# Kernel tuning notes

Measured on AMD Instinct MI355X. Metric: run time of the kernel, lower is better.

## Reference

```python
import jax, jax.numpy as jnp
import numpy as np

N, S, R, CM = 1, 128, 256, 256
C, CZ = 32, 128


def setup_inputs() -> dict:
    key = jax.random.key(0)
    k1, k2, k3, k4 = jax.random.split(key, 4)
    return {
        "msa_repr": jax.random.normal(k1, (N, S, R, CM), dtype=jnp.float32),
        "left_proj": jax.random.normal(k2, (CM, C), dtype=jnp.float32) * 0.05,
        "right_proj": jax.random.normal(k3, (CM, C), dtype=jnp.float32) * 0.05,
        "out_proj": jax.random.normal(k4, (C * C, CZ), dtype=jnp.float32) * 0.05,
    }


def reference(msa_repr, left_proj, right_proj, out_proj):
    # msa_repr: [N, S, R, CM]
    # Project to left/right activations and move R before S
    # (equivalent to torch matmul + transpose(-2, -3)).
    a = jnp.einsum("nsrm,mc->nrsc", msa_repr, left_proj)   # [N, R, S, C]
    b = jnp.einsum("nsrm,mc->nrsc", msa_repr, right_proj)  # [N, R, S, C]
    # Outer product contracted over the MSA dim S:
    # outer[n, r, t, c, e] = sum_s a[n, r, s, c] * b[n, t, s, e]
    outer = jnp.einsum("nrsc,ntse->nrtce", a, b)            # [N, R, R, C, C]
    n, r, t = outer.shape[:3]
    outer = outer.reshape(n, r, t, C * C)                   # [N, R, R, C*C]
    # Output projection to pair channels cz
    return outer @ out_proj                                 # [N, R, R, CZ]
```

## Files before the change

kernel.cpp:

```cpp
#include <hip/hip_runtime.h>

typedef __bf16 bf16x8 __attribute__((ext_vector_type(8)));
typedef __bf16 bf16x4 __attribute__((ext_vector_type(4)));
typedef float f32x16 __attribute__((ext_vector_type(16)));

constexpr int S = 128, R = 256, CM = 256, C = 32, CZ = 128;

#define MFMA __builtin_amdgcn_mfma_f32_32x32x16_bf16

__device__ __forceinline__ bf16x4 cvt4(float a, float b, float c, float d) {
    bf16x4 r;
    r[0] = (__bf16)a; r[1] = (__bf16)b; r[2] = (__bf16)c; r[3] = (__bf16)d;
    return r;
}

__global__ __launch_bounds__(256) void k_wt(const float* __restrict__ W,
                                            __bf16* __restrict__ WTf) {
    int g = blockIdx.x * 256 + threadIdx.x;
    int cz = g & 127;
    int k = g >> 7;
    int e = k >> 5, c = k & 31;
    float v = W[(size_t)(c * 32 + e) * 128 + cz];
    WTf[((size_t)(k >> 3) * 128 + cz) * 8 + (k & 7)] = (__bf16)v;
}

__global__ __launch_bounds__(256) void k_wlr(const float* __restrict__ Lp,
                                             const float* __restrict__ Rp,
                                             __bf16* __restrict__ WLRT) {
    int c = blockIdx.x;
    int m = threadIdx.x;
    const float* src = (c < 32) ? Lp : Rp;
    WLRT[(size_t)c * 256 + m] = (__bf16)src[(size_t)m * 32 + (c & 31)];
}

__global__ __launch_bounds__(256) void k_proj(const float* __restrict__ msa,
                                              const __bf16* __restrict__ WLRT,
                                              __bf16* __restrict__ aTf,
                                              __bf16* __restrict__ bTf) {
    __shared__ __align__(16) __bf16 As[128 * 256];
    const int r = blockIdx.x;
    const int t = threadIdx.x;
    const int w = t >> 6;
    const int lane = t & 63;

#pragma unroll 4
    for (int it = 0; it < 32; ++it) {
        int row = it * 4 + w;
        float4 v = *(const float4*)&msa[((size_t)row * R + r) * CM + lane * 4];
        bf16x4 h = cvt4(v.x, v.y, v.z, v.w);
        int P = (lane >> 1) ^ (row & 15);
        *(bf16x4*)((char*)As + row * 512 + P * 16 + (lane & 1) * 8) = h;
    }
    __syncthreads();

    const int l31 = t & 31;
    const int kh = (t >> 5) & 1;
    f32x16 accL, accR;
#pragma unroll
    for (int q = 0; q < 16; ++q) { accL[q] = 0.f; accR[q] = 0.f; }

    const bf16x8* wbL = (const bf16x8*)&WLRT[(size_t)l31 * 256 + 8 * kh];
    const bf16x8* wbR = (const bf16x8*)&WLRT[(size_t)(32 + l31) * 256 + 8 * kh];
    const int srow = w * 32 + l31;
    const char* arow = (const char*)As + srow * 512;

    __builtin_amdgcn_s_setprio(1);
#pragma unroll
    for (int ks = 0; ks < 16; ++ks) {
        int P = (2 * ks + kh) ^ (srow & 15);
        bf16x8 af = *(const bf16x8*)(arow + P * 16);
        accL = MFMA(af, wbL[2 * ks], accL, 0, 0, 0);
        accR = MFMA(af, wbR[2 * ks], accR, 0, 0, 0);
    }
    __builtin_amdgcn_s_setprio(0);

#pragma unroll
    for (int q = 0; q < 4; ++q) {
        size_t base = (size_t)r * 4096 + (size_t)(2 * w + (q >> 1)) * 512 +
                      (size_t)(q & 1) * 256 + (size_t)l31 * 8 + 4 * kh;
        *(bf16x4*)&aTf[base] = cvt4(accL[4 * q + 0], accL[4 * q + 1],
                                    accL[4 * q + 2], accL[4 * q + 3]);
        *(bf16x4*)&bTf[base] = cvt4(accR[4 * q + 0], accR[4 * q + 1],
                                    accR[4 * q + 2], accR[4 * q + 3]);
    }
}

__global__ __launch_bounds__(256, 2) void k_main(const __bf16* __restrict__ aTf,
                                                 const __bf16* __restrict__ bTf,
                                                 const __bf16* __restrict__ WTf,
                                                 float* __restrict__ out) {
    __shared__ __align__(16) __bf16 Gs[32 * 1024];

    const int t = threadIdx.x;
    const int w = t >> 6;
    const int l = t & 63;
    const int lane = l & 31;
    const int kh = l >> 5;
    const int r0 = blockIdx.x * 8;
    const int t0 = blockIdx.y * 4;

    f32x16 acc[2][4];
#pragma unroll
    for (int i = 0; i < 2; ++i)
#pragma unroll
        for (int j = 0; j < 4; ++j)
#pragma unroll
            for (int q = 0; q < 16; ++q) acc[i][j][q] = 0.f;

    const bf16x8* ap0 = (const bf16x8*)aTf + ((size_t)(r0 + 2 * w + 0) * 512 + kh * 32 + lane);
    const bf16x8* ap1 = (const bf16x8*)aTf + ((size_t)(r0 + 2 * w + 1) * 512 + kh * 32 + lane);
    const bf16x8* bp0 = (const bf16x8*)bTf + ((size_t)(t0 + 0) * 512 + kh * 32 + lane);
    const bf16x8* bp1 = (const bf16x8*)bTf + ((size_t)(t0 + 1) * 512 + kh * 32 + lane);
    const bf16x8* bp2 = (const bf16x8*)bTf + ((size_t)(t0 + 2) * 512 + kh * 32 + lane);
    const bf16x8* bp3 = (const bf16x8*)bTf + ((size_t)(t0 + 3) * 512 + kh * 32 + lane);

    bf16x8 A0[2], B0[4], A1[2], B1[4], A2[2], B2[4];
#define LDA(Aa, Bb, ks) do { \
    Aa[0] = ap0[(ks) * 64]; Aa[1] = ap1[(ks) * 64]; \
    Bb[0] = bp0[(ks) * 64]; Bb[1] = bp1[(ks) * 64]; \
    Bb[2] = bp2[(ks) * 64]; Bb[3] = bp3[(ks) * 64]; } while (0)
#define PH_A(Aa, Bb) do { \
    __builtin_amdgcn_s_setprio(1); \
    acc[0][0] = MFMA(Aa[0], Bb[0], acc[0][0], 0, 0, 0); \
    acc[0][1] = MFMA(Aa[0], Bb[1], acc[0][1], 0, 0, 0); \
    acc[0][2] = MFMA(Aa[0], Bb[2], acc[0][2], 0, 0, 0); \
    acc[0][3] = MFMA(Aa[0], Bb[3], acc[0][3], 0, 0, 0); \
    acc[1][0] = MFMA(Aa[1], Bb[0], acc[1][0], 0, 0, 0); \
    acc[1][1] = MFMA(Aa[1], Bb[1], acc[1][1], 0, 0, 0); \
    acc[1][2] = MFMA(Aa[1], Bb[2], acc[1][2], 0, 0, 0); \
    acc[1][3] = MFMA(Aa[1], Bb[3], acc[1][3], 0, 0, 0); \
    __builtin_amdgcn_s_setprio(0); } while (0)

    LDA(A0, B0, 0); LDA(A1, B1, 1); LDA(A2, B2, 2);
    PH_A(A0, B0); LDA(A0, B0, 3);
    PH_A(A1, B1); LDA(A1, B1, 4);
    PH_A(A2, B2); LDA(A2, B2, 5);
    PH_A(A0, B0); LDA(A0, B0, 6);
    PH_A(A1, B1); LDA(A1, B1, 7);
    PH_A(A2, B2);
    PH_A(A0, B0);
    PH_A(A1, B1);

#pragma unroll
    for (int i = 0; i < 2; ++i) {
#pragma unroll
        for (int j = 0; j < 4; ++j) {
            int p = (2 * w + i) * 4 + j;
            unsigned prow = (unsigned)p * 2048;
#pragma unroll
            for (int q = 0; q < 4; ++q) {
                int Lc = lane * 4 + q;
                int P = Lc ^ (p & 15) ^ (lane & 7);
                *(bf16x4*)((char*)Gs + prow + (unsigned)P * 16 + kh * 8) =
                    cvt4(acc[i][j][4 * q + 0], acc[i][j][4 * q + 1],
                         acc[i][j][4 * q + 2], acc[i][j][4 * q + 3]);
            }
        }
    }
    __syncthreads();

    f32x16 oA, oB;
#pragma unroll
    for (int q = 0; q < 16; ++q) { oA[q] = 0.f; oB[q] = 0.f; }

    const int czl = w * 32 + lane;
    const bf16x8* wb = (const bf16x8*)WTf + ((size_t)kh * 128 + czl);
    const unsigned prow = (unsigned)lane * 2048;
    const int p15 = lane & 15;

#define LDG1(dst, kk) do { \
    int Lr = (kk) * 2 + kh; \
    int P = Lr ^ p15 ^ ((Lr >> 2) & 7); \
    dst = *(const bf16x8*)((const char*)Gs + prow + (unsigned)P * 16); } while (0)

    bf16x8 G0[8], G1[8], W0[8], W1[8], W2[8];
#define LDG8(Gg, kb) do { \
    LDG1(Gg[0], (kb) + 0); LDG1(Gg[1], (kb) + 1); LDG1(Gg[2], (kb) + 2); LDG1(Gg[3], (kb) + 3); \
    LDG1(Gg[4], (kb) + 4); LDG1(Gg[5], (kb) + 5); LDG1(Gg[6], (kb) + 6); LDG1(Gg[7], (kb) + 7); } while (0)
#define LDW8(Ww, kb) do { \
    Ww[0] = wb[((kb) + 0) * 256]; Ww[1] = wb[((kb) + 1) * 256]; \
    Ww[2] = wb[((kb) + 2) * 256]; Ww[3] = wb[((kb) + 3) * 256]; \
    Ww[4] = wb[((kb) + 4) * 256]; Ww[5] = wb[((kb) + 5) * 256]; \
    Ww[6] = wb[((kb) + 6) * 256]; Ww[7] = wb[((kb) + 7) * 256]; } while (0)
#define PH_B(Gg, Ww) do { \
    __builtin_amdgcn_s_setprio(1); \
    oA = MFMA(Gg[0], Ww[0], oA, 0, 0, 0); oB = MFMA(Gg[1], Ww[1], oB, 0, 0, 0); \
    oA = MFMA(Gg[2], Ww[2], oA, 0, 0, 0); oB = MFMA(Gg[3], Ww[3], oB, 0, 0, 0); \
    oA = MFMA(Gg[4], Ww[4], oA, 0, 0, 0); oB = MFMA(Gg[5], Ww[5], oB, 0, 0, 0); \
    oA = MFMA(Gg[6], Ww[6], oA, 0, 0, 0); oB = MFMA(Gg[7], Ww[7], oB, 0, 0, 0); \
    __builtin_amdgcn_s_setprio(0); } while (0)

    LDW8(W0, 0); LDW8(W1, 8); LDW8(W2, 16);
    LDG8(G0, 0); LDG8(G1, 8);
    PH_B(G0, W0); LDW8(W0, 24); LDG8(G0, 16);
    PH_B(G1, W1); LDW8(W1, 32); LDG8(G1, 24);
    PH_B(G0, W2); LDW8(W2, 40); LDG8(G0, 32);
    PH_B(G1, W0); LDW8(W0, 48); LDG8(G1, 40);
    PH_B(G0, W1); LDW8(W1, 56); LDG8(G0, 48);
    PH_B(G1, W2);                LDG8(G1, 56);
    PH_B(G0, W0);
    PH_B(G1, W1);

    f32x16 o = oA + oB;

#pragma unroll
    for (int reg = 0; reg < 16; ++reg) {
        int p = (reg & 3) + 8 * (reg >> 2) + 4 * kh;
        int pr = p >> 2, pt = p & 3;
        out[((size_t)(r0 + pr) * 256 + (t0 + pt)) * 128 + czl] = o[reg];
    }
}

extern "C" void kernel_launch(void* const* d_in, const int* in_sizes, int n_in,
                              void* d_out, int out_size, void* d_ws, size_t ws_size,
                              hipStream_t stream) {
    const float* msa = (const float*)d_in[0];
    const float* left = (const float*)d_in[1];
    const float* right = (const float*)d_in[2];
    const float* W = (const float*)d_in[3];

    __bf16* aTf = (__bf16*)d_ws;
    __bf16* bTf = aTf + (size_t)R * 4096;
    __bf16* WTf = bTf + (size_t)R * 4096;
    __bf16* WLRT = WTf + (size_t)128 * 1024;
    float* outp = (float*)d_out;

    k_wt<<<512, 256, 0, stream>>>(W, WTf);
    k_wlr<<<64, 256, 0, stream>>>(left, right, WLRT);
    k_proj<<<256, 256, 0, stream>>>(msa, WLRT, aTf, bTf);
    k_main<<<dim3(32, 64), 256, 0, stream>>>(aTf, bTf, WTf, outp);
}
```

Measured before the change: 67.20 us.

## Enlarge main tile to 8x8 pairs with split-K output projection and LDS reduction

k_main now uses 512-thread blocks covering 8 r by 8 t pairs, which halves the grid and reuses each loaded a row across twice as many t columns. The output projection is split over K across wave pairs, each wave computing a 2x2 block of 32x32 MFMA tiles, and the partial sums are combined through an fp32 LDS reduction. k_proj is split across two S halves so it launches twice as many blocks, each computing a single projection per wave. The aim is more reuse of the W and G operands and better parallelism, at the cost of more LDS traffic and extra barriers for the reduction.

```diff
diff --git a/kernel.cpp b/kernel.cpp
--- a/kernel.cpp
+++ b/kernel.cpp
@@ -3,6 +3,7 @@
 typedef __bf16 bf16x8 __attribute__((ext_vector_type(8)));
 typedef __bf16 bf16x4 __attribute__((ext_vector_type(4)));
 typedef float f32x16 __attribute__((ext_vector_type(16)));
+typedef float f32x4 __attribute__((ext_vector_type(4)));
 
 constexpr int S = 128, R = 256, CM = 256, C = 32, CZ = 128;
 
@@ -37,31 +38,35 @@
                                               const __bf16* __restrict__ WLRT,
                                               __bf16* __restrict__ aTf,
                                               __bf16* __restrict__ bTf) {
-    __shared__ __align__(16) __bf16 As[128 * 256];
+    __shared__ __align__(16) __bf16 As[64 * 256];
     const int r = blockIdx.x;
+    const int sh = blockIdx.y;
     const int t = threadIdx.x;
+
+#pragma unroll 4
+    for (int it = 0; it < 16; ++it) {
+        int idx = it * 256 + t;
+        int row = idx >> 6;
+        int cg = idx & 63;
+        float4 v = *(const float4*)&msa[((size_t)(sh * 64 + row) * R + r) * CM + cg * 4];
+        bf16x4 h = cvt4(v.x, v.y, v.z, v.w);
+        int P = (cg >> 1) ^ (row & 15);
+        *(bf16x4*)((char*)As + row * 512 + P * 16 + (cg & 1) * 8) = h;
+    }
+    __syncthreads();
+
     const int w = t >> 6;
-    const int lane = t & 63;
-
-#pragma unroll 4
-    for (int it = 0; it < 32; ++it) {
-        int row = it * 4 + w;
-        float4 v = *(const float4*)&msa[((size_t)row * R + r) * CM + lane * 4];
-        bf16x4 h = cvt4(v.x, v.y, v.z, v.w);
-        int P = (lane >> 1) ^ (row & 15);
-        *(bf16x4*)((char*)As + row * 512 + P * 16 + (lane & 1) * 8) = h;
-    }
-    __syncthreads();
-
     const int l31 = t & 31;
     const int kh = (t >> 5) & 1;
-    f32x16 accL, accR;
-#pragma unroll
-    for (int q = 0; q < 16; ++q) { accL[q] = 0.f; accR[q] = 0.f; }
-
-    const bf16x8* wbL = (const bf16x8*)&WLRT[(size_t)l31 * 256 + 8 * kh];
-    const bf16x8* wbR = (const bf16x8*)&WLRT[(size_t)(32 + l31) * 256 + 8 * kh];
-    const int srow = w * 32 + l31;
+    const int sd = w & 1;
+    const int mi = w >> 1;
+
+    f32x16 acc;
+#pragma unroll
+    for (int q = 0; q < 16; ++q) acc[q] = 0.f;
+
+    const bf16x8* wb = (const bf16x8*)&WLRT[(size_t)(sd * 32 + l31) * 256 + 8 * kh];
+    const int srow = mi * 32 + l31;
     const char* arow = (const char*)As + srow * 512;
 
     __builtin_amdgcn_s_setprio(1);
@@ -69,27 +74,26 @@
     for (int ks = 0; ks < 16; ++ks) {
         int P = (2 * ks + kh) ^ (srow & 15);
         bf16x8 af = *(const bf16x8*)(arow + P * 16);
-        accL = MFMA(af, wbL[2 * ks], accL, 0, 0, 0);
-        accR = MFMA(af, wbR[2 * ks], accR, 0, 0, 0);
+        acc = MFMA(af, wb[2 * ks], acc, 0, 0, 0);
     }
     __builtin_amdgcn_s_setprio(0);
 
+    __bf16* dst = sd ? bTf : aTf;
+    const int wg = sh * 2 + mi;
 #pragma unroll
     for (int q = 0; q < 4; ++q) {
-        size_t base = (size_t)r * 4096 + (size_t)(2 * w + (q >> 1)) * 512 +
+        size_t base = (size_t)r * 4096 + (size_t)(2 * wg + (q >> 1)) * 512 +
                       (size_t)(q & 1) * 256 + (size_t)l31 * 8 + 4 * kh;
-        *(bf16x4*)&aTf[base] = cvt4(accL[4 * q + 0], accL[4 * q + 1],
-                                    accL[4 * q + 2], accL[4 * q + 3]);
-        *(bf16x4*)&bTf[base] = cvt4(accR[4 * q + 0], accR[4 * q + 1],
-                                    accR[4 * q + 2], accR[4 * q + 3]);
-    }
-}
-
-__global__ __launch_bounds__(256, 2) void k_main(const __bf16* __restrict__ aTf,
+        *(bf16x4*)&dst[base] = cvt4(acc[4 * q + 0], acc[4 * q + 1],
+                                    acc[4 * q + 2], acc[4 * q + 3]);
+    }
+}
+
+__global__ __launch_bounds__(512, 2) void k_main(const __bf16* __restrict__ aTf,
                                                  const __bf16* __restrict__ bTf,
                                                  const __bf16* __restrict__ WTf,
                                                  float* __restrict__ out) {
-    __shared__ __align__(16) __bf16 Gs[32 * 1024];
+    __shared__ __align__(16) __bf16 Gs[64 * 1024];
 
     const int t = threadIdx.x;
     const int w = t >> 6;
@@ -97,7 +101,10 @@
     const int lane = l & 31;
     const int kh = l >> 5;
     const int r0 = blockIdx.x * 8;
-    const int t0 = blockIdx.y * 4;
+    const int t0 = blockIdx.y * 8;
+
+    const int rg = w >> 1;
+    const int tg = w & 1;
 
     f32x16 acc[2][4];
 #pragma unroll
@@ -107,14 +114,14 @@
 #pragma unroll
             for (int q = 0; q < 16; ++q) acc[i][j][q] = 0.f;
 
-    const bf16x8* ap0 = (const bf16x8*)aTf + ((size_t)(r0 + 2 * w + 0) * 512 + kh * 32 + lane);
-    const bf16x8* ap1 = (const bf16x8*)aTf + ((size_t)(r0 + 2 * w + 1) * 512 + kh * 32 + lane);
-    const bf16x8* bp0 = (const bf16x8*)bTf + ((size_t)(t0 + 0) * 512 + kh * 32 + lane);
-    const bf16x8* bp1 = (const bf16x8*)bTf + ((size_t)(t0 + 1) * 512 + kh * 32 + lane);
-    const bf16x8* bp2 = (const bf16x8*)bTf + ((size_t)(t0 + 2) * 512 + kh * 32 + lane);
-    const bf16x8* bp3 = (const bf16x8*)bTf + ((size_t)(t0 + 3) * 512 + kh * 32 + lane);
-
-    bf16x8 A0[2], B0[4], A1[2], B1[4], A2[2], B2[4];
+    const bf16x8* ap0 = (const bf16x8*)aTf + ((size_t)(r0 + 2 * rg + 0) * 512 + kh * 32 + lane);
+    const bf16x8* ap1 = (const bf16x8*)aTf + ((size_t)(r0 + 2 * rg + 1) * 512 + kh * 32 + lane);
+    const bf16x8* bp0 = (const bf16x8*)bTf + ((size_t)(t0 + 4 * tg + 0) * 512 + kh * 32 + lane);
+    const bf16x8* bp1 = (const bf16x8*)bTf + ((size_t)(t0 + 4 * tg + 1) * 512 + kh * 32 + lane);
+    const bf16x8* bp2 = (const bf16x8*)bTf + ((size_t)(t0 + 4 * tg + 2) * 512 + kh * 32 + lane);
+    const bf16x8* bp3 = (const bf16x8*)bTf + ((size_t)(t0 + 4 * tg + 3) * 512 + kh * 32 + lane);
+
+    bf16x8 A0[2], B0[4], A1[2], B1[4];
 #define LDA(Aa, Bb, ks) do { \
     Aa[0] = ap0[(ks) * 64]; Aa[1] = ap1[(ks) * 64]; \
     Bb[0] = bp0[(ks) * 64]; Bb[1] = bp1[(ks) * 64]; \
@@ -131,21 +138,20 @@
     acc[1][3] = MFMA(Aa[1], Bb[3], acc[1][3], 0, 0, 0); \
     __builtin_amdgcn_s_setprio(0); } while (0)
 
-    LDA(A0, B0, 0); LDA(A1, B1, 1); LDA(A2, B2, 2);
-    PH_A(A0, B0); LDA(A0, B0, 3);
-    PH_A(A1, B1); LDA(A1, B1, 4);
-    PH_A(A2, B2); LDA(A2, B2, 5);
-    PH_A(A0, B0); LDA(A0, B0, 6);
-    PH_A(A1, B1); LDA(A1, B1, 7);
-    PH_A(A2, B2);
-    PH_A(A0, B0);
-    PH_A(A1, B1);
+    LDA(A0, B0, 0);
+#pragma unroll
+    for (int ks = 0; ks < 8; ks += 2) {
+        LDA(A1, B1, ks + 1);
+        PH_A(A0, B0);
+        LDA(A0, B0, (ks + 2) & 7);
+        PH_A(A1, B1);
+    }
 
 #pragma unroll
     for (int i = 0; i < 2; ++i) {
 #pragma unroll
         for (int j = 0; j < 4; ++j) {
-            int p = (2 * w + i) * 4 + j;
+            int p = (2 * rg + i) * 8 + 4 * tg + j;
             unsigned prow = (unsigned)p * 2048;
 #pragma unroll
             for (int q = 0; q < 4; ++q) {
@@ -159,55 +165,88 @@
     }
     __syncthreads();
 
-    f32x16 oA, oB;
-#pragma unroll
-    for (int q = 0; q < 16; ++q) { oA[q] = 0.f; oB[q] = 0.f; }
-
-    const int czl = w * 32 + lane;
-    const bf16x8* wb = (const bf16x8*)WTf + ((size_t)kh * 128 + czl);
-    const unsigned prow = (unsigned)lane * 2048;
+    const int kq = w >> 1;
+    const int ng = w & 1;
+    const int czl0 = ng * 64 + lane;
+    const int czl1 = czl0 + 32;
+    const bf16x8* wb0 = (const bf16x8*)WTf + ((size_t)kh * 128 + czl0);
+    const bf16x8* wb1 = (const bf16x8*)WTf + ((size_t)kh * 128 + czl1);
+    const unsigned prow0 = (unsigned)lane * 2048;
+    const unsigned prow1 = (unsigned)(lane + 32) * 2048;
     const int p15 = lane & 15;
 
-#define LDG1(dst, kk) do { \
+    f32x16 o00, o01, o10, o11;
+#pragma unroll
+    for (int q = 0; q < 16; ++q) { o00[q] = 0.f; o01[q] = 0.f; o10[q] = 0.f; o11[q] = 0.f; }
+
+    bf16x8 Wa0, Wa1, Ga0, Ga1, Wb0_, Wb1_, Gb0, Gb1;
+#define LDB(W0v, W1v, G0v, G1v, kk) do { \
+    W0v = wb0[(size_t)(kk) * 256]; \
+    W1v = wb1[(size_t)(kk) * 256]; \
     int Lr = (kk) * 2 + kh; \
     int P = Lr ^ p15 ^ ((Lr >> 2) & 7); \
-    dst = *(const bf16x8*)((const char*)Gs + prow + (unsigned)P * 16); } while (0)
-
-    bf16x8 G0[8], G1[8], W0[8], W1[8], W2[8];
-#define LDG8(Gg, kb) do { \
-    LDG1(Gg[0], (kb) + 0); LDG1(Gg[1], (kb) + 1); LDG1(Gg[2], (kb) + 2); LDG1(Gg[3], (kb) + 3); \
-    LDG1(Gg[4], (kb) + 4); LDG1(Gg[5], (kb) + 5); LDG1(Gg[6], (kb) + 6); LDG1(Gg[7], (kb) + 7); } while (0)
-#define LDW8(Ww, kb) do { \
-    Ww[0] = wb[((kb) + 0) * 256]; Ww[1] = wb[((kb) + 1) * 256]; \
-    Ww[2] = wb[((kb) + 2) * 256]; Ww[3] = wb[((kb) + 3) * 256]; \
-    Ww[4] = wb[((kb) + 4) * 256]; Ww[5] = wb[((kb) + 5) * 256]; \
-    Ww[6] = wb[((kb) + 6) * 256]; Ww[7] = wb[((kb) + 7) * 256]; } while (0)
-#define PH_B(Gg, Ww) do { \
+    G0v = *(const bf16x8*)((const char*)Gs + prow0 + (unsigned)P * 16); \
+    G1v = *(const bf16x8*)((const char*)Gs + prow1 + (unsigned)P * 16); } while (0)
+#define PHB(W0v, W1v, G0v, G1v) do { \
     __builtin_amdgcn_s_setprio(1); \
-    oA = MFMA(Gg[0], Ww[0], oA, 0, 0, 0); oB = MFMA(Gg[1], Ww[1], oB, 0, 0, 0); \
-    oA = MFMA(Gg[2], Ww[2], oA, 0, 0, 0); oB = MFMA(Gg[3], Ww[3], oB, 0, 0, 0); \
-    oA = MFMA(Gg[4], Ww[4], oA, 0, 0, 0); oB = MFMA(Gg[5], Ww[5], oB, 0, 0, 0); \
-    oA = MFMA(Gg[6], Ww[6], oA, 0, 0, 0); oB = MFMA(Gg[7], Ww[7], oB, 0, 0, 0); \
+    o00 = MFMA(G0v, W0v, o00, 0, 0, 0); \
+    o01 = MFMA(G0v, W1v, o01, 0, 0, 0); \
+    o10 = MFMA(G1v, W0v, o10, 0, 0, 0); \
+    o11 = MFMA(G1v, W1v, o11, 0, 0, 0); \
     __builtin_amdgcn_s_setprio(0); } while (0)
 
-    LDW8(W0, 0); LDW8(W1, 8); LDW8(W2, 16);
-    LDG8(G0, 0); LDG8(G1, 8);
-    PH_B(G0, W0); LDW8(W0, 24); LDG8(G0, 16);
-    PH_B(G1, W1); LDW8(W1, 32); LDG8(G1, 24);
-    PH_B(G0, W2); LDW8(W2, 40); LDG8(G0, 32);
-    PH_B(G1, W0); LDW8(W0, 48); LDG8(G1, 40);
-    PH_B(G0, W1); LDW8(W1, 56); LDG8(G0, 48);
-    PH_B(G1, W2);                LDG8(G1, 56);
-    PH_B(G0, W0);
-    PH_B(G1, W1);
-
-    f32x16 o = oA + oB;
-
-#pragma unroll
-    for (int reg = 0; reg < 16; ++reg) {
-        int p = (reg & 3) + 8 * (reg >> 2) + 4 * kh;
-        int pr = p >> 2, pt = p & 3;
-        out[((size_t)(r0 + pr) * 256 + (t0 + pt)) * 128 + czl] = o[reg];
+    LDB(Wa0, Wa1, Ga0, Ga1, kq * 16);
+#pragma unroll
+    for (int j = 0; j < 16; j += 2) {
+        LDB(Wb0_, Wb1_, Gb0, Gb1, kq * 16 + ((j + 1) & 15));
+        PHB(Wa0, Wa1, Ga0, Ga1);
+        LDB(Wa0, Wa1, Ga0, Ga1, kq * 16 + ((j + 2) & 15));
+        PHB(Wb0_, Wb1_, Gb0, Gb1);
+    }
+    __syncthreads();
+
+    {
+        char* pr = (char*)Gs + (size_t)w * 16384;
+        const f32x16* os[4] = {&o00, &o01, &o10, &o11};
+#pragma unroll
+        for (int s2 = 0; s2 < 4; ++s2) {
+#pragma unroll
+            for (int pc = 0; pc < 4; ++pc) {
+                f32x4 v;
+                v[0] = (*os[s2])[4 * pc + 0]; v[1] = (*os[s2])[4 * pc + 1];
+                v[2] = (*os[s2])[4 * pc + 2]; v[3] = (*os[s2])[4 * pc + 3];
+                *(f32x4*)(pr + ((s2 * 4 + pc) * 64 + l) * 16) = v;
+            }
+        }
+    }
+    __syncthreads();
+
+    {
+        const int ngx = w >> 2;
+        const int mix = (w >> 1) & 1;
+        const int nix = w & 1;
+        const int s2 = mix * 2 + nix;
+        f32x16 sm;
+#pragma unroll
+        for (int q = 0; q < 16; ++q) sm[q] = 0.f;
+#pragma unroll
+        for (int kq2 = 0; kq2 < 4; ++kq2) {
+            const char* pr = (const char*)Gs + (size_t)(kq2 * 2 + ngx) * 16384;
+#pragma unroll
+            for (int pc = 0; pc < 4; ++pc) {
+                f32x4 v = *(const f32x4*)(pr + ((s2 * 4 + pc) * 64 + l) * 16);
+                sm[4 * pc + 0] += v[0]; sm[4 * pc + 1] += v[1];
+                sm[4 * pc + 2] += v[2]; sm[4 * pc + 3] += v[3];
+            }
+        }
+        const int czl = ngx * 64 + nix * 32 + (l & 31);
+        const int khx = l >> 5;
+#pragma unroll
+        for (int reg = 0; reg < 16; ++reg) {
+            int pl = mix * 32 + (reg & 3) + 8 * (reg >> 2) + 4 * khx;
+            int prr = pl >> 3, ptt = pl & 7;
+            out[((size_t)(r0 + prr) * 256 + (t0 + ptt)) * 128 + czl] = sm[reg];
+        }
     }
 }
 
@@ -227,6 +266,6 @@
 
     k_wt<<<512, 256, 0, stream>>>(W, WTf);
     k_wlr<<<64, 256, 0, stream>>>(left, right, WLRT);
-    k_proj<<<256, 256, 0, stream>>>(msa, WLRT, aTf, bTf);
-    k_main<<<dim3(32, 64), 256, 0, stream>>>(aTf, bTf, WTf, outp);
-}
+    k_proj<<<dim3(256, 2), 256, 0, stream>>>(msa, WLRT, aTf, bTf);
+    k_main<<<dim3(32, 32), 512, 0, stream>>>(aTf, bTf, WTf, outp);
+}
```

Measured after the change: 60.61 us. 1.11x faster.
